# Optimization experiments

Measured on AMD Instinct MI355X. Metric: run time of the kernel, lower is better.

Reference implementation:

```python
import jax, jax.numpy as jnp
import numpy as np

N = 100000      # nodes
E = 600000      # directed edges (before self-loops)
NFEAT = 128
NHID = 128
NCLASS = 64


def setup_inputs() -> dict:
    key = jax.random.key(0)
    k1, k2, k3, k4 = jax.random.split(key, 4)
    x = jax.random.normal(k1, (N, NFEAT), dtype=jnp.float32)
    edge_index = jax.random.randint(k2, (2, E), 0, N, dtype=jnp.int32)
    # GCNConv learned params (Glorot-ish init), bias zeros as in PyG default
    W1 = jax.random.normal(k3, (NFEAT, NHID), dtype=jnp.float32) / jnp.sqrt(NFEAT)
    b1 = jnp.zeros((NHID,), dtype=jnp.float32)
    W2 = jax.random.normal(k4, (NHID, NCLASS), dtype=jnp.float32) / jnp.sqrt(NHID)
    b2 = jnp.zeros((NCLASS,), dtype=jnp.float32)
    return {"x": x, "edge_index": edge_index, "W1": W1, "b1": b1, "W2": W2, "b2": b2}


def _gcn_layer(x, src, dst, norm, W, b, n):
    # PyG GCNConv: linear transform, then normalized neighbor aggregation, then bias
    h = x @ W                                   # [N, out]
    msg = h[src] * norm[:, None]                # [E+N, out] gather + scale
    agg = jax.ops.segment_sum(msg, dst, num_segments=n)  # scatter-add
    return agg + b


def reference(x, edge_index, W1, b1, W2, b2):
    n = x.shape[0]
    # add self-loops (PyG gcn_norm default add_self_loops=True)
    loops = jnp.arange(n, dtype=edge_index.dtype)
    src = jnp.concatenate([edge_index[0], loops])
    dst = jnp.concatenate([edge_index[1], loops])
    # symmetric normalization: D^-1/2 (A+I) D^-1/2
    deg = jax.ops.segment_sum(jnp.ones_like(dst, dtype=x.dtype), dst, num_segments=n)
    d_inv_sqrt = jnp.where(deg > 0, jax.lax.rsqrt(deg), 0.0)
    norm = d_inv_sqrt[src] * d_inv_sqrt[dst]
    h = jax.nn.relu(_gcn_layer(x, src, dst, norm, W1, b1, n))
    # F.dropout with training=False is identity -> omitted in eval reference
    return _gcn_layer(h, src, dst, norm, W2, b2, n)
```

## Files before the change

kernel.cpp:

```cpp
#include <hip/hip_runtime.h>


typedef unsigned short u16;
typedef unsigned int u32;
typedef __attribute__((ext_vector_type(8))) short bf16x8;
typedef __attribute__((ext_vector_type(4))) float f32x4;

#define BSH 9
#define BMSK ((1 << BSH) - 1)
#define MAXBK 256
#define SEG 2560
#define HISTB 128

__device__ __forceinline__ u16 f2b(float f) {
  u32 u = __float_as_uint(f);
  u32 r = (u + 0x7FFFu + ((u >> 16) & 1u)) >> 16;
  return (u16)r;
}
__device__ __forceinline__ u32 pk2(float a, float b) {
  return (u32)f2b(a) | ((u32)f2b(b) << 16);
}
__device__ __forceinline__ void dec8(uint4 v, float f[8]) {
  f[0] = __uint_as_float(v.x << 16);
  f[1] = __uint_as_float(v.x & 0xFFFF0000u);
  f[2] = __uint_as_float(v.y << 16);
  f[3] = __uint_as_float(v.y & 0xFFFF0000u);
  f[4] = __uint_as_float(v.z << 16);
  f[5] = __uint_as_float(v.z & 0xFFFF0000u);
  f[6] = __uint_as_float(v.w << 16);
  f[7] = __uint_as_float(v.w & 0xFFFF0000u);
}
__device__ __forceinline__ void fma8(uint4 v, float d, float acc[8]) {
  acc[0] = fmaf(__uint_as_float(v.x << 16), d, acc[0]);
  acc[1] = fmaf(__uint_as_float(v.x & 0xFFFF0000u), d, acc[1]);
  acc[2] = fmaf(__uint_as_float(v.y << 16), d, acc[2]);
  acc[3] = fmaf(__uint_as_float(v.y & 0xFFFF0000u), d, acc[3]);
  acc[4] = fmaf(__uint_as_float(v.z << 16), d, acc[4]);
  acc[5] = fmaf(__uint_as_float(v.z & 0xFFFF0000u), d, acc[5]);
  acc[6] = fmaf(__uint_as_float(v.w << 16), d, acc[6]);
  acc[7] = fmaf(__uint_as_float(v.w & 0xFFFF0000u), d, acc[7]);
}


__global__ __launch_bounds__(256) void prep_hist_k(const void* __restrict__ W1,
                                                   const void* __restrict__ b1,
                                                   const void* __restrict__ W2,
                                                   const void* __restrict__ b2,
                                                   u16* __restrict__ W1b, u16* __restrict__ ob1,
                                                   u16* __restrict__ W2t, u16* __restrict__ ob2,
                                                   int* __restrict__ mode,
                                                   const int* __restrict__ dst,
                                                   int* __restrict__ bhist,
                                                   int E, int PREPB) {
  const int tid = threadIdx.x;

  if ((int)blockIdx.x >= PREPB) {
    __shared__ int lh[MAXBK];
    const int hb = (int)blockIdx.x - PREPB;
    for (int j = tid; j < MAXBK; j += 256) lh[j] = 0;
    __syncthreads();
    const int chunk = (E + HISTB - 1) / HISTB;
    const int e0 = hb * chunk;
    const int e1 = min(E, e0 + chunk);
    for (int e = e0 + tid; e < e1; e += 256) atomicAdd(&lh[dst[e] >> BSH], 1);
    __syncthreads();
    for (int j = tid; j < MAXBK; j += 256) {
      int v = lh[j];
      if (v) atomicAdd(&bhist[j], v);
    }
    return;
  }

  __shared__ int cnt_s;
  if (tid == 0) cnt_s = 0;
  __syncthreads();
  int c = 0;
  for (int j = tid; j < 4096; j += 256) {
    u32 e = (((const u16*)W1)[j] >> 7) & 0xFFu;
    if (e >= 100u && e <= 130u) c++;
  }
  atomicAdd(&cnt_s, c);
  __syncthreads();
  const int m = (cnt_s < 3328) ? 1 : 0;
  if (blockIdx.x == 0 && tid == 0) *mode = m;

  int i = blockIdx.x * 256 + tid;
  if (i < 24768) {
    int j = i;
    const void* src;
    u16* dstp;
    int sidx, didx;
    if (j < 16384) {
      src = W1; dstp = W1b; sidx = j; didx = j;
    } else if ((j -= 16384) < 128) {
      src = b1; dstp = ob1; sidx = j; didx = j;
    } else if ((j -= 128) < 8192) {
      int nn = j >> 7, k = j & 127;
      src = W2; dstp = W2t; sidx = k * 64 + nn; didx = j;
    } else {
      j -= 8192;
      src = b2; dstp = ob2; sidx = j; didx = j;
    }
    dstp[didx] = m ? f2b(((const float*)src)[sidx]) : ((const u16*)src)[sidx];
  }
}


__global__ __launch_bounds__(256) void part_k(const int* __restrict__ src,
                                              const int* __restrict__ dst,
                                              const int* __restrict__ bhist,
                                              int* __restrict__ boff,
                                              int2* __restrict__ tmp,
                                              int E, int NBK) {
  __shared__ int ls[SEG];
  __shared__ int ld_[SEG];
  __shared__ int lh[MAXBK];
  __shared__ int base_[MAXBK];
  __shared__ int bsl[MAXBK];
  const int tid = threadIdx.x;

  int ov = (tid < NBK) ? bhist[tid] : 0;
  bsl[tid] = ov;
  __syncthreads();
#pragma unroll
  for (int off = 1; off < 256; off <<= 1) {
    int add = (tid >= off) ? bsl[tid - off] : 0;
    __syncthreads();
    bsl[tid] += add;
    __syncthreads();
  }
  bsl[tid] -= ov;
  if (tid < MAXBK) lh[tid] = 0;
  __syncthreads();

  const int e0 = blockIdx.x * SEG;
  const int len = min(SEG, E - e0);
  for (int j = tid; j < len; j += 256) {
    int s = src[e0 + j];
    int d = dst[e0 + j];
    ls[j] = s;
    ld_[j] = d;
    atomicAdd(&lh[d >> BSH], 1);
  }
  __syncthreads();
  if (tid < NBK) {
    int hh = lh[tid];
    base_[tid] = hh ? bsl[tid] + atomicAdd(&boff[tid], hh) : 0;
    lh[tid] = 0;
  }
  __syncthreads();
  for (int j = tid; j < len; j += 256) {
    int d = ld_[j];
    int bk = d >> BSH;
    int r = atomicAdd(&lh[bk], 1);
    tmp[base_[bk] + r] = make_int2(ls[j], d);
  }
}


__global__ __launch_bounds__(256) void nbuild_k(const int2* __restrict__ tmp,
                                                const int* __restrict__ bhist,
                                                float* __restrict__ dinv,
                                                int4* __restrict__ ninfo,
                                                int* __restrict__ spI,
                                                int np, int NBK) {
  __shared__ int bsl[MAXBK];
  __shared__ int cntl[1 << BSH];
  __shared__ int curl[1 << BSH];
  __shared__ int sc2[256];
  const int tid = threadIdx.x;
  const int b = blockIdx.x;

  int ov = (tid < NBK) ? bhist[tid] : 0;
  bsl[tid] = ov;
  __syncthreads();
#pragma unroll
  for (int off = 1; off < 256; off <<= 1) {
    int add = (tid >= off) ? bsl[tid - off] : 0;
    __syncthreads();
    bsl[tid] += add;
    __syncthreads();
  }
  bsl[tid] -= ov;
  cntl[tid] = 0;
  cntl[tid + 256] = 0;
  curl[tid] = 0;
  curl[tid + 256] = 0;
  __syncthreads();

  const int bs = bsl[b];
  const int be = bs + bhist[b];
  const int lo = b << BSH;

  for (int e = bs + tid; e < be; e += 256) {
    int2 p = tmp[e];
    atomicAdd(&cntl[p.y & BMSK], 1);
  }
  __syncthreads();

  const int c0 = cntl[2 * tid];
  const int c1 = cntl[2 * tid + 1];
  const int s2 = c0 + c1;
  sc2[tid] = s2;
  __syncthreads();
#pragma unroll
  for (int off = 1; off < 256; off <<= 1) {
    int add = (tid >= off) ? sc2[tid - off] : 0;
    __syncthreads();
    sc2[tid] += add;
    __syncthreads();
  }
  const int excl = sc2[tid] - s2;
  const int e0n = excl;
  const int e1n = excl + c0;

  {
    int i0 = lo + 2 * tid;
    if (i0 < np) {
      float dv = rsqrtf((float)c0 + 1.0f);
      dinv[i0] = dv;
      ninfo[i0] = make_int4(bs + e0n, c0, __float_as_int(dv), 0);
    }
    int i1 = i0 + 1;
    if (i1 < np) {
      float dv = rsqrtf((float)c1 + 1.0f);
      dinv[i1] = dv;
      ninfo[i1] = make_int4(bs + e1n, c1, __float_as_int(dv), 0);
    }
  }
  cntl[2 * tid] = e0n;
  cntl[2 * tid + 1] = e1n;
  __syncthreads();

  for (int e = bs + tid; e < be; e += 256) {
    int2 p = tmp[e];
    int loc = p.y & BMSK;
    int r = atomicAdd(&curl[loc], 1);
    spI[bs + cntl[loc] + r] = p.x;
  }
}


__global__ __launch_bounds__(256) void gemm1_k(const void* __restrict__ Araw,
                                               const u16* __restrict__ W,
                                               u16* __restrict__ out, int M,
                                               const int* __restrict__ mode) {
  __shared__ __align__(16) u16 Wt[128 * 136];
  __shared__ __align__(16) u16 As[64 * 136];
  const int tid = threadIdx.x;
  const int mcv = *mode;

  for (int idx = tid; idx < 128 * 128; idx += 256) {
    int n = idx & 127;
    int k = idx >> 7;
    Wt[n * 136 + k] = W[k * 128 + n];
  }
  __syncthreads();

  const int wv = tid >> 6, lane = tid & 63, lr = lane & 15, lq = lane >> 4;
  const int ntiles = (M + 63) >> 6;

  for (int t = blockIdx.x; t < ntiles; t += gridDim.x) {
    const int r0 = t * 64;
    __syncthreads();
    for (int idx = tid; idx < 64 * 16; idx += 256) {
      int row = idx >> 4, c = idx & 15;
      uint4 v = make_uint4(0u, 0u, 0u, 0u);
      if (r0 + row < M) {
        if (mcv) {
          const float* xf = (const float*)Araw + (size_t)(r0 + row) * 128 + c * 8;
          float4 f0 = *(const float4*)xf;
          float4 f1 = *(const float4*)(xf + 4);
          v.x = pk2(f0.x, f0.y);
          v.y = pk2(f0.z, f0.w);
          v.z = pk2(f1.x, f1.y);
          v.w = pk2(f1.z, f1.w);
        } else {
          v = *(const uint4*)((const u16*)Araw + (size_t)(r0 + row) * 128 + c * 8);
        }
      }
      *(uint4*)&As[row * 136 + c * 8] = v;
    }
    __syncthreads();

    bf16x8 a[4];
#pragma unroll
    for (int s = 0; s < 4; ++s)
      a[s] = *(const bf16x8*)&As[(wv * 16 + lr) * 136 + s * 32 + lq * 8];

#pragma unroll
    for (int nt = 0; nt < 8; ++nt) {
      f32x4 acc = {0.f, 0.f, 0.f, 0.f};
#pragma unroll
      for (int s = 0; s < 4; ++s) {
        bf16x8 b = *(const bf16x8*)&Wt[(nt * 16 + lr) * 136 + s * 32 + lq * 8];
        acc = __builtin_amdgcn_mfma_f32_16x16x32_bf16(a[s], b, acc, 0, 0, 0);
      }
#pragma unroll
      for (int r = 0; r < 4; ++r) {
        int row = r0 + wv * 16 + lq * 4 + r;
        if (row < M) out[(size_t)row * 128 + nt * 16 + lr] = f2b(acc[r]);
      }
    }
  }
}


__global__ __launch_bounds__(256) void fusedB_k(const u16* __restrict__ h,
                                                const int* __restrict__ spI,
                                                const int4* __restrict__ ninfo,
                                                const float* __restrict__ dinv,
                                                const u16* __restrict__ b1,
                                                const u16* __restrict__ W2t,
                                                u16* __restrict__ g, int n) {
  __shared__ __align__(16) u16 As[16 * 136];
  const int tid = threadIdx.x, wv = tid >> 6, lane = tid & 63;
  const int lq = lane >> 4, lr = lane & 15;
  const int base = blockIdx.x * 16;
  const int i = base + wv * 4 + lq;
  const bool valid = (i < n);

  int start = 0, c = 0;
  float di = 0.f;
  if (valid) {
    int4 ni = ninfo[i];
    start = ni.x;
    c = ni.y;
    di = __int_as_float(ni.z);
  }
  float acc[8];
  {
    uint4 v = valid ? *(const uint4*)(h + (size_t)i * 128 + lr * 8)
                    : make_uint4(0u, 0u, 0u, 0u);
    float f[8];
    dec8(v, f);
#pragma unroll
    for (int j = 0; j < 8; ++j) acc[j] = f[j] * di;
  }
  const int bl = lq * 16;
  for (int bs = 0; __any(bs < c); bs += 16) {
    int m = c - bs;
    m = m < 0 ? 0 : (m > 16 ? 16 : m);
    int s = 0;
    float dv = 0.f;
    if (lr < m) {
      s = spI[start + bs + lr];
      dv = dinv[s];
    }
    int mmw = m;
    mmw = max(mmw, __shfl_xor(mmw, 16));
    mmw = max(mmw, __shfl_xor(mmw, 32));
    for (int e = 0; e < mmw; e += 4) {
      int s0 = __shfl(s, bl + e), s1 = __shfl(s, bl + e + 1);
      int s2 = __shfl(s, bl + e + 2), s3 = __shfl(s, bl + e + 3);
      float d0 = __shfl(dv, bl + e);
      float d1 = __shfl(dv, bl + e + 1);
      float d2 = __shfl(dv, bl + e + 2);
      float d3 = __shfl(dv, bl + e + 3);
      uint4 v0 = *(const uint4*)(h + (size_t)s0 * 128 + lr * 8);
      uint4 v1 = *(const uint4*)(h + (size_t)s1 * 128 + lr * 8);
      uint4 v2 = *(const uint4*)(h + (size_t)s2 * 128 + lr * 8);
      uint4 v3 = *(const uint4*)(h + (size_t)s3 * 128 + lr * 8);
      fma8(v0, d0, acc);
      fma8(v1, d1, acc);
      fma8(v2, d2, acc);
      fma8(v3, d3, acc);
    }
  }
  {
    uint4 bv = *(const uint4*)(b1 + lr * 8);
    float bf[8];
    dec8(bv, bf);
    float o[8];
#pragma unroll
    for (int j = 0; j < 8; ++j) o[j] = fmaxf(fmaf(acc[j], di, bf[j]), 0.f);
    uint4 ov;
    ov.x = pk2(o[0], o[1]);
    ov.y = pk2(o[2], o[3]);
    ov.z = pk2(o[4], o[5]);
    ov.w = pk2(o[6], o[7]);
    *(uint4*)&As[(wv * 4 + lq) * 136 + lr * 8] = ov;
  }
  __syncthreads();

  bf16x8 a[4];
#pragma unroll
  for (int s = 0; s < 4; ++s)
    a[s] = *(const bf16x8*)&As[lr * 136 + s * 32 + lq * 8];
  {
    const int nt = wv;
    f32x4 acc4 = {0.f, 0.f, 0.f, 0.f};
#pragma unroll
    for (int s = 0; s < 4; ++s) {
      bf16x8 b = *(const bf16x8*)&W2t[(nt * 16 + lr) * 128 + s * 32 + lq * 8];
      acc4 = __builtin_amdgcn_mfma_f32_16x16x32_bf16(a[s], b, acc4, 0, 0, 0);
    }
#pragma unroll
    for (int r = 0; r < 4; ++r) {
      int row = base + lq * 4 + r;
      if (row < n) g[(size_t)row * 64 + nt * 16 + lr] = f2b(acc4[r]);
    }
  }
}


__global__ __launch_bounds__(256) void agg2_k(const u16* __restrict__ g,
                                              const int* __restrict__ spI,
                                              const int4* __restrict__ ninfo,
                                              const float* __restrict__ dinv,
                                              const u16* __restrict__ b2,
                                              void* __restrict__ outv, int n,
                                              const int* __restrict__ mode) {
  const int lane = threadIdx.x & 63;
  const int o8 = lane >> 3, l8 = lane & 7;
  const int i = blockIdx.x * 32 + (threadIdx.x >> 6) * 8 + o8;
  const bool valid = (i < n);

  int start = 0, c = 0;
  float di = 0.f;
  if (valid) {
    int4 ni = ninfo[i];
    start = ni.x;
    c = ni.y;
    di = __int_as_float(ni.z);
  }
  float acc[8];
  {
    uint4 v = valid ? *(const uint4*)(g + (size_t)i * 64 + l8 * 8)
                    : make_uint4(0u, 0u, 0u, 0u);
    float f[8];
    dec8(v, f);
#pragma unroll
    for (int j = 0; j < 8; ++j) acc[j] = f[j] * di;
  }
  const int bl = o8 * 8;
  for (int base = 0; __any(base < c); base += 8) {
    int m = c - base;
    m = m < 0 ? 0 : (m > 8 ? 8 : m);
    int s = 0;
    float dv = 0.f;
    if (l8 < m) {
      s = spI[start + base + l8];
      dv = dinv[s];
    }
    int mmw = m;
    mmw = max(mmw, __shfl_xor(mmw, 8));
    mmw = max(mmw, __shfl_xor(mmw, 16));
    mmw = max(mmw, __shfl_xor(mmw, 32));
    for (int e = 0; e < mmw; e += 4) {
      int s0 = __shfl(s, bl + e), s1 = __shfl(s, bl + e + 1);
      int s2 = __shfl(s, bl + e + 2), s3 = __shfl(s, bl + e + 3);
      float d0 = __shfl(dv, bl + e);
      float d1 = __shfl(dv, bl + e + 1);
      float d2 = __shfl(dv, bl + e + 2);
      float d3 = __shfl(dv, bl + e + 3);
      uint4 v0 = *(const uint4*)(g + (size_t)s0 * 64 + l8 * 8);
      uint4 v1 = *(const uint4*)(g + (size_t)s1 * 64 + l8 * 8);
      uint4 v2 = *(const uint4*)(g + (size_t)s2 * 64 + l8 * 8);
      uint4 v3 = *(const uint4*)(g + (size_t)s3 * 64 + l8 * 8);
      fma8(v0, d0, acc);
      fma8(v1, d1, acc);
      fma8(v2, d2, acc);
      fma8(v3, d3, acc);
    }
  }
  if (valid) {
    uint4 bv = *(const uint4*)(b2 + l8 * 8);
    float bf[8];
    dec8(bv, bf);
    float o[8];
#pragma unroll
    for (int j = 0; j < 8; ++j) o[j] = fmaf(acc[j], di, bf[j]);
    if (*mode) {
      float* op = (float*)outv + (size_t)i * 64 + l8 * 8;
      *(float4*)op = make_float4(o[0], o[1], o[2], o[3]);
      *(float4*)(op + 4) = make_float4(o[4], o[5], o[6], o[7]);
    } else {
      uint4 ov;
      ov.x = pk2(o[0], o[1]);
      ov.y = pk2(o[2], o[3]);
      ov.z = pk2(o[4], o[5]);
      ov.w = pk2(o[6], o[7]);
      *(uint4*)((u16*)outv + (size_t)i * 64 + l8 * 8) = ov;
    }
  }
}


extern "C" void kernel_launch(void* const* d_in, const int* in_sizes, int n_in,
                              void* d_out, int out_size, void* d_ws, size_t ws_size,
                              hipStream_t stream) {
  const void* x_raw  = d_in[0];
  const int*  ei     = (const int*)d_in[1];
  const void* W1_raw = d_in[2];
  const void* b1_raw = d_in[3];
  const void* W2_raw = d_in[4];
  const void* b2_raw = d_in[5];

  const int N = in_sizes[0] / 128;
  const int E = in_sizes[1] / 2;
  const int NP = ((N + 255) / 256) * 256;
  const int NBK = (NP + (1 << BSH) - 1) >> BSH;
  const int PREPB = (24768 + 255) / 256;

  char* ws = (char*)d_ws;
  size_t off = 0;
  auto alloc = [&](size_t bytes) -> void* {
    void* p = ws + off;
    off = (off + bytes + 255) & ~(size_t)255;
    return p;
  };
  int*   mode    = (int*)alloc(4);
  int*   bz      = (int*)alloc((size_t)2 * MAXBK * 4);
  int*   bhist   = bz;
  int*   boff    = bz + MAXBK;
  float* dinv    = (float*)alloc((size_t)NP * 4);
  int4*  ninfo   = (int4*)alloc((size_t)NP * 16);
  int*   spI     = (int*)alloc((size_t)E * 4);
  int2*  tmp     = (int2*)alloc((size_t)E * 8);
  u16*   W1b     = (u16*)alloc((size_t)128 * 128 * 2);
  u16*   b1b     = (u16*)alloc(128 * 2);
  u16*   W2t     = (u16*)alloc((size_t)64 * 128 * 2);
  u16*   b2b     = (u16*)alloc(64 * 2);
  u16*   h       = (u16*)alloc((size_t)N * 128 * 2);
  u16*   g       = (u16*)alloc((size_t)N * 64 * 2);

  const int pb = (E + SEG - 1) / SEG;

  hipMemsetAsync(bz, 0, (size_t)2 * MAXBK * 4, stream);
  prep_hist_k<<<PREPB + HISTB, 256, 0, stream>>>(W1_raw, b1_raw, W2_raw, b2_raw,
                                                 W1b, b1b, W2t, b2b, mode,
                                                 ei + E, bhist, E, PREPB);
  part_k<<<pb, 256, 0, stream>>>(ei, ei + E, bhist, boff, tmp, E, NBK);
  nbuild_k<<<NBK, 256, 0, stream>>>(tmp, bhist, dinv, ninfo, spI, NP, NBK);
  gemm1_k<<<512, 256, 0, stream>>>(x_raw, W1b, h, N, mode);
  fusedB_k<<<(N + 15) / 16, 256, 0, stream>>>(h, spI, ninfo, dinv, b1b, W2t, g, N);
  agg2_k<<<(N + 31) / 32, 256, 0, stream>>>(g, spI, ninfo, dinv, b2b, d_out, N, mode);
}
```

Before: 194.4 us.

## Sort nodes by degree to balance per-wave work in aggregation kernels

Builds a degree histogram in nbuild_k, then uses extra blocks in the GEMM launch to counting-sort node ids by in-degree into a permutation. The two aggregation kernels process nodes in this permuted order, so the lanes of a wave handle nodes with similar neighbor counts and diverge less. The cost is an extra histogram and scatter pass, an indirect perm lookup, and scattered output row writes in place of contiguous ones.

```diff
diff --git a/kernel.cpp b/kernel.cpp
--- a/kernel.cpp
+++ b/kernel.cpp
@@ -11,6 +11,7 @@
 #define MAXBK 256
 #define SEG 2560
 #define HISTB 128
+#define GEMMB 512
 
 __device__ __forceinline__ u16 f2b(float f) {
   u32 u = __float_as_uint(f);
@@ -163,7 +164,8 @@
                                                 float* __restrict__ dinv,
                                                 int4* __restrict__ ninfo,
                                                 int* __restrict__ spI,
-                                                int np, int NBK) {
+                                                int* __restrict__ dhist,
+                                                int np, int n, int NBK) {
   __shared__ int bsl[MAXBK];
   __shared__ int cntl[1 << BSH];
   __shared__ int curl[1 << BSH];
@@ -220,12 +222,14 @@
       float dv = rsqrtf((float)c0 + 1.0f);
       dinv[i0] = dv;
       ninfo[i0] = make_int4(bs + e0n, c0, __float_as_int(dv), 0);
+      if (i0 < n) atomicAdd(&dhist[min(c0, 255)], 1);
     }
     int i1 = i0 + 1;
     if (i1 < np) {
       float dv = rsqrtf((float)c1 + 1.0f);
       dinv[i1] = dv;
       ninfo[i1] = make_int4(bs + e1n, c1, __float_as_int(dv), 0);
+      if (i1 < n) atomicAdd(&dhist[min(c1, 255)], 1);
     }
   }
   cntl[2 * tid] = e0n;
@@ -241,13 +245,57 @@
 }
 
 
-__global__ __launch_bounds__(256) void gemm1_k(const void* __restrict__ Araw,
-                                               const u16* __restrict__ W,
-                                               u16* __restrict__ out, int M,
-                                               const int* __restrict__ mode) {
+__global__ __launch_bounds__(256) void gemmperm_k(const void* __restrict__ Araw,
+                                                  const u16* __restrict__ W,
+                                                  u16* __restrict__ out, int M,
+                                                  const int* __restrict__ mode,
+                                                  const int4* __restrict__ ninfo,
+                                                  const int* __restrict__ dhist,
+                                                  int* __restrict__ dcur,
+                                                  int* __restrict__ perm,
+                                                  int NBp) {
   __shared__ __align__(16) u16 Wt[128 * 136];
   __shared__ __align__(16) u16 As[64 * 136];
+  __shared__ int lh[256];
+  __shared__ int base_[256];
+  __shared__ int dbase[256];
   const int tid = threadIdx.x;
+
+  if ((int)blockIdx.x < NBp) {
+    int ov = dhist[tid];
+    dbase[tid] = ov;
+    __syncthreads();
+#pragma unroll
+    for (int off = 1; off < 256; off <<= 1) {
+      int add = (tid >= off) ? dbase[tid - off] : 0;
+      __syncthreads();
+      dbase[tid] += add;
+      __syncthreads();
+    }
+    dbase[tid] -= ov;
+    lh[tid] = 0;
+    __syncthreads();
+
+    const int i = blockIdx.x * 256 + tid;
+    int c = -1;
+    if (i < M) {
+      c = min(ninfo[i].y, 255);
+      atomicAdd(&lh[c], 1);
+    }
+    __syncthreads();
+    {
+      int hh = lh[tid];
+      base_[tid] = hh ? dbase[tid] + atomicAdd(&dcur[tid], hh) : 0;
+      lh[tid] = 0;
+    }
+    __syncthreads();
+    if (i < M) {
+      int r = atomicAdd(&lh[c], 1);
+      perm[base_[c] + r] = i;
+    }
+    return;
+  }
+
   const int mcv = *mode;
 
   for (int idx = tid; idx < 128 * 128; idx += 256) {
@@ -260,7 +308,7 @@
   const int wv = tid >> 6, lane = tid & 63, lr = lane & 15, lq = lane >> 4;
   const int ntiles = (M + 63) >> 6;
 
-  for (int t = blockIdx.x; t < ntiles; t += gridDim.x) {
+  for (int t = (int)blockIdx.x - NBp; t < ntiles; t += GEMMB) {
     const int r0 = t * 64;
     __syncthreads();
     for (int idx = tid; idx < 64 * 16; idx += 256) {
@@ -310,15 +358,19 @@
                                                 const int* __restrict__ spI,
                                                 const int4* __restrict__ ninfo,
                                                 const float* __restrict__ dinv,
+                                                const int* __restrict__ perm,
                                                 const u16* __restrict__ b1,
                                                 const u16* __restrict__ W2t,
                                                 u16* __restrict__ g, int n) {
   __shared__ __align__(16) u16 As[16 * 136];
+  __shared__ int pids[16];
   const int tid = threadIdx.x, wv = tid >> 6, lane = tid & 63;
   const int lq = lane >> 4, lr = lane & 15;
   const int base = blockIdx.x * 16;
-  const int i = base + wv * 4 + lq;
-  const bool valid = (i < n);
+  const int idx = base + wv * 4 + lq;
+  const bool valid = (idx < n);
+  const int i = valid ? perm[idx] : -1;
+  if (lr == 0) pids[wv * 4 + lq] = i;
 
   int start = 0, c = 0;
   float di = 0.f;
@@ -397,8 +449,8 @@
     }
 #pragma unroll
     for (int r = 0; r < 4; ++r) {
-      int row = base + lq * 4 + r;
-      if (row < n) g[(size_t)row * 64 + nt * 16 + lr] = f2b(acc4[r]);
+      int row = pids[lq * 4 + r];
+      if (row >= 0) g[(size_t)row * 64 + nt * 16 + lr] = f2b(acc4[r]);
     }
   }
 }
@@ -408,13 +460,15 @@
                                               const int* __restrict__ spI,
                                               const int4* __restrict__ ninfo,
                                               const float* __restrict__ dinv,
+                                              const int* __restrict__ perm,
                                               const u16* __restrict__ b2,
                                               void* __restrict__ outv, int n,
                                               const int* __restrict__ mode) {
   const int lane = threadIdx.x & 63;
   const int o8 = lane >> 3, l8 = lane & 7;
-  const int i = blockIdx.x * 32 + (threadIdx.x >> 6) * 8 + o8;
-  const bool valid = (i < n);
+  const int idx = blockIdx.x * 32 + (threadIdx.x >> 6) * 8 + o8;
+  const bool valid = (idx < n);
+  const int i = valid ? perm[idx] : 0;
 
   int start = 0, c = 0;
   float di = 0.f;
@@ -502,6 +556,7 @@
   const int NP = ((N + 255) / 256) * 256;
   const int NBK = (NP + (1 << BSH) - 1) >> BSH;
   const int PREPB = (24768 + 255) / 256;
+  const int NBp = (N + 255) / 256;
 
   char* ws = (char*)d_ws;
   size_t off = 0;
@@ -511,12 +566,15 @@
     return p;
   };
   int*   mode    = (int*)alloc(4);
-  int*   bz      = (int*)alloc((size_t)2 * MAXBK * 4);
+  int*   bz      = (int*)alloc((size_t)(2 * MAXBK + 512) * 4);
   int*   bhist   = bz;
   int*   boff    = bz + MAXBK;
+  int*   dhist   = bz + 2 * MAXBK;
+  int*   dcur    = bz + 2 * MAXBK + 256;
   float* dinv    = (float*)alloc((size_t)NP * 4);
   int4*  ninfo   = (int4*)alloc((size_t)NP * 16);
   int*   spI     = (int*)alloc((size_t)E * 4);
+  int*   perm    = (int*)alloc((size_t)NP * 4);
   int2*  tmp     = (int2*)alloc((size_t)E * 8);
   u16*   W1b     = (u16*)alloc((size_t)128 * 128 * 2);
   u16*   b1b     = (u16*)alloc(128 * 2);
@@ -527,13 +585,14 @@
 
   const int pb = (E + SEG - 1) / SEG;
 
-  hipMemsetAsync(bz, 0, (size_t)2 * MAXBK * 4, stream);
+  hipMemsetAsync(bz, 0, (size_t)(2 * MAXBK + 512) * 4, stream);
   prep_hist_k<<<PREPB + HISTB, 256, 0, stream>>>(W1_raw, b1_raw, W2_raw, b2_raw,
                                                  W1b, b1b, W2t, b2b, mode,
                                                  ei + E, bhist, E, PREPB);
   part_k<<<pb, 256, 0, stream>>>(ei, ei + E, bhist, boff, tmp, E, NBK);
-  nbuild_k<<<NBK, 256, 0, stream>>>(tmp, bhist, dinv, ninfo, spI, NP, NBK);
-  gemm1_k<<<512, 256, 0, stream>>>(x_raw, W1b, h, N, mode);
-  fusedB_k<<<(N + 15) / 16, 256, 0, stream>>>(h, spI, ninfo, dinv, b1b, W2t, g, N);
-  agg2_k<<<(N + 31) / 32, 256, 0, stream>>>(g, spI, ninfo, dinv, b2b, d_out, N, mode);
-}
+  nbuild_k<<<NBK, 256, 0, stream>>>(tmp, bhist, dinv, ninfo, spI, dhist, NP, N, NBK);
+  gemmperm_k<<<NBp + GEMMB, 256, 0, stream>>>(x_raw, W1b, h, N, mode,
+                                              ninfo, dhist, dcur, perm, NBp);
+  fusedB_k<<<(N + 15) / 16, 256, 0, stream>>>(h, spI, ninfo, dinv, perm, b1b, W2t, g, N);
+  agg2_k<<<(N + 31) / 32, 256, 0, stream>>>(g, spI, ninfo, dinv, perm, b2b, d_out, N, mode);
+}
```

Result: slower. 568.4 us (+192.4%).

## Merge CSR build and first GEMM into one launch; load A fragments directly

Applied to the files above, without the earlier changes.

The neighbor-list build kernel and the first-layer GEMM are merged into a single launch. The first NBK blocks do the per-bucket CSR construction, reusing the weight shared-memory buffer as integer scratch, and the remaining blocks run the GEMM, so the two independent stages overlap and one launch is removed. The GEMM also drops the shared-memory staging of A tiles and its block barriers, loading each lane's bf16 fragments straight from global memory. The direct loads are less coalesced than the staged copy.

```diff
diff --git a/kernel.cpp b/kernel.cpp
--- a/kernel.cpp
+++ b/kernel.cpp
@@ -11,6 +11,7 @@
 #define MAXBK 256
 #define SEG 2560
 #define HISTB 128
+#define GEMMB 512
 
 __device__ __forceinline__ u16 f2b(float f) {
   u32 u = __float_as_uint(f);
@@ -158,96 +159,97 @@
 }
 
 
-__global__ __launch_bounds__(256) void nbuild_k(const int2* __restrict__ tmp,
+__global__ __launch_bounds__(256) void nbgemm_k(const int2* __restrict__ tmp,
                                                 const int* __restrict__ bhist,
                                                 float* __restrict__ dinv,
                                                 int4* __restrict__ ninfo,
                                                 int* __restrict__ spI,
-                                                int np, int NBK) {
-  __shared__ int bsl[MAXBK];
-  __shared__ int cntl[1 << BSH];
-  __shared__ int curl[1 << BSH];
-  __shared__ int sc2[256];
+                                                int np, int NBK,
+                                                const void* __restrict__ Araw,
+                                                const u16* __restrict__ W,
+                                                u16* __restrict__ hout, int M,
+                                                const int* __restrict__ mode) {
+  __shared__ __align__(16) u16 Wt[128 * 136];
   const int tid = threadIdx.x;
-  const int b = blockIdx.x;
-
-  int ov = (tid < NBK) ? bhist[tid] : 0;
-  bsl[tid] = ov;
-  __syncthreads();
-#pragma unroll
-  for (int off = 1; off < 256; off <<= 1) {
-    int add = (tid >= off) ? bsl[tid - off] : 0;
-    __syncthreads();
-    bsl[tid] += add;
-    __syncthreads();
-  }
-  bsl[tid] -= ov;
-  cntl[tid] = 0;
-  cntl[tid + 256] = 0;
-  curl[tid] = 0;
-  curl[tid + 256] = 0;
-  __syncthreads();
-
-  const int bs = bsl[b];
-  const int be = bs + bhist[b];
-  const int lo = b << BSH;
-
-  for (int e = bs + tid; e < be; e += 256) {
-    int2 p = tmp[e];
-    atomicAdd(&cntl[p.y & BMSK], 1);
-  }
-  __syncthreads();
-
-  const int c0 = cntl[2 * tid];
-  const int c1 = cntl[2 * tid + 1];
-  const int s2 = c0 + c1;
-  sc2[tid] = s2;
-  __syncthreads();
-#pragma unroll
-  for (int off = 1; off < 256; off <<= 1) {
-    int add = (tid >= off) ? sc2[tid - off] : 0;
-    __syncthreads();
-    sc2[tid] += add;
-    __syncthreads();
-  }
-  const int excl = sc2[tid] - s2;
-  const int e0n = excl;
-  const int e1n = excl + c0;
-
-  {
-    int i0 = lo + 2 * tid;
-    if (i0 < np) {
-      float dv = rsqrtf((float)c0 + 1.0f);
-      dinv[i0] = dv;
-      ninfo[i0] = make_int4(bs + e0n, c0, __float_as_int(dv), 0);
-    }
-    int i1 = i0 + 1;
-    if (i1 < np) {
-      float dv = rsqrtf((float)c1 + 1.0f);
-      dinv[i1] = dv;
-      ninfo[i1] = make_int4(bs + e1n, c1, __float_as_int(dv), 0);
-    }
-  }
-  cntl[2 * tid] = e0n;
-  cntl[2 * tid + 1] = e1n;
-  __syncthreads();
-
-  for (int e = bs + tid; e < be; e += 256) {
-    int2 p = tmp[e];
-    int loc = p.y & BMSK;
-    int r = atomicAdd(&curl[loc], 1);
-    spI[bs + cntl[loc] + r] = p.x;
-  }
-}
-
-
-__global__ __launch_bounds__(256) void gemm1_k(const void* __restrict__ Araw,
-                                               const u16* __restrict__ W,
-                                               u16* __restrict__ out, int M,
-                                               const int* __restrict__ mode) {
-  __shared__ __align__(16) u16 Wt[128 * 136];
-  __shared__ __align__(16) u16 As[64 * 136];
-  const int tid = threadIdx.x;
+
+  if ((int)blockIdx.x < NBK) {
+    int* ibuf = (int*)Wt;
+    int* bsl  = ibuf;
+    int* cntl = ibuf + 256;
+    int* curl = ibuf + 768;
+    int* sc2  = ibuf + 1280;
+    const int b = blockIdx.x;
+
+    int ov = (tid < NBK) ? bhist[tid] : 0;
+    bsl[tid] = ov;
+    __syncthreads();
+#pragma unroll
+    for (int off = 1; off < 256; off <<= 1) {
+      int add = (tid >= off) ? bsl[tid - off] : 0;
+      __syncthreads();
+      bsl[tid] += add;
+      __syncthreads();
+    }
+    bsl[tid] -= ov;
+    cntl[tid] = 0;
+    cntl[tid + 256] = 0;
+    curl[tid] = 0;
+    curl[tid + 256] = 0;
+    __syncthreads();
+
+    const int bs = bsl[b];
+    const int be = bs + bhist[b];
+    const int lo = b << BSH;
+
+    for (int e = bs + tid; e < be; e += 256) {
+      int2 p = tmp[e];
+      atomicAdd(&cntl[p.y & BMSK], 1);
+    }
+    __syncthreads();
+
+    const int c0 = cntl[2 * tid];
+    const int c1 = cntl[2 * tid + 1];
+    const int s2 = c0 + c1;
+    sc2[tid] = s2;
+    __syncthreads();
+#pragma unroll
+    for (int off = 1; off < 256; off <<= 1) {
+      int add = (tid >= off) ? sc2[tid - off] : 0;
+      __syncthreads();
+      sc2[tid] += add;
+      __syncthreads();
+    }
+    const int excl = sc2[tid] - s2;
+    const int e0n = excl;
+    const int e1n = excl + c0;
+
+    {
+      int i0 = lo + 2 * tid;
+      if (i0 < np) {
+        float dv = rsqrtf((float)c0 + 1.0f);
+        dinv[i0] = dv;
+        ninfo[i0] = make_int4(bs + e0n, c0, __float_as_int(dv), 0);
+      }
+      int i1 = i0 + 1;
+      if (i1 < np) {
+        float dv = rsqrtf((float)c1 + 1.0f);
+        dinv[i1] = dv;
+        ninfo[i1] = make_int4(bs + e1n, c1, __float_as_int(dv), 0);
+      }
+    }
+    cntl[2 * tid] = e0n;
+    cntl[2 * tid + 1] = e1n;
+    __syncthreads();
+
+    for (int e = bs + tid; e < be; e += 256) {
+      int2 p = tmp[e];
+      int loc = p.y & BMSK;
+      int r = atomicAdd(&curl[loc], 1);
+      spI[bs + cntl[loc] + r] = p.x;
+    }
+    return;
+  }
+
   const int mcv = *mode;
 
   for (int idx = tid; idx < 128 * 128; idx += 256) {
@@ -260,33 +262,35 @@
   const int wv = tid >> 6, lane = tid & 63, lr = lane & 15, lq = lane >> 4;
   const int ntiles = (M + 63) >> 6;
 
-  for (int t = blockIdx.x; t < ntiles; t += gridDim.x) {
+  for (int t = (int)blockIdx.x - NBK; t < ntiles; t += GEMMB) {
     const int r0 = t * 64;
-    __syncthreads();
-    for (int idx = tid; idx < 64 * 16; idx += 256) {
-      int row = idx >> 4, c = idx & 15;
-      uint4 v = make_uint4(0u, 0u, 0u, 0u);
-      if (r0 + row < M) {
-        if (mcv) {
-          const float* xf = (const float*)Araw + (size_t)(r0 + row) * 128 + c * 8;
-          float4 f0 = *(const float4*)xf;
-          float4 f1 = *(const float4*)(xf + 4);
-          v.x = pk2(f0.x, f0.y);
-          v.y = pk2(f0.z, f0.w);
-          v.z = pk2(f1.x, f1.y);
-          v.w = pk2(f1.z, f1.w);
-        } else {
-          v = *(const uint4*)((const u16*)Araw + (size_t)(r0 + row) * 128 + c * 8);
+    const int arow = r0 + wv * 16 + lr;
+    const bool rok = (arow < M);
+
+    bf16x8 a[4];
+    if (mcv) {
+      const float* xr = (const float*)Araw + (size_t)arow * 128 + lq * 8;
+#pragma unroll
+      for (int s = 0; s < 4; ++s) {
+        uint4 u = make_uint4(0u, 0u, 0u, 0u);
+        if (rok) {
+          float4 f0 = *(const float4*)(xr + s * 32);
+          float4 f1 = *(const float4*)(xr + s * 32 + 4);
+          u.x = pk2(f0.x, f0.y);
+          u.y = pk2(f0.z, f0.w);
+          u.z = pk2(f1.x, f1.y);
+          u.w = pk2(f1.z, f1.w);
         }
+        a[s] = *(const bf16x8*)&u;
       }
-      *(uint4*)&As[row * 136 + c * 8] = v;
-    }
-    __syncthreads();
-
-    bf16x8 a[4];
-#pragma unroll
-    for (int s = 0; s < 4; ++s)
-      a[s] = *(const bf16x8*)&As[(wv * 16 + lr) * 136 + s * 32 + lq * 8];
+    } else {
+      const u16* xr = (const u16*)Araw + (size_t)arow * 128 + lq * 8;
+#pragma unroll
+      for (int s = 0; s < 4; ++s) {
+        uint4 u = rok ? *(const uint4*)(xr + s * 32) : make_uint4(0u, 0u, 0u, 0u);
+        a[s] = *(const bf16x8*)&u;
+      }
+    }
 
 #pragma unroll
     for (int nt = 0; nt < 8; ++nt) {
@@ -299,7 +303,7 @@
 #pragma unroll
       for (int r = 0; r < 4; ++r) {
         int row = r0 + wv * 16 + lq * 4 + r;
-        if (row < M) out[(size_t)row * 128 + nt * 16 + lr] = f2b(acc[r]);
+        if (row < M) hout[(size_t)row * 128 + nt * 16 + lr] = f2b(acc[r]);
       }
     }
   }
@@ -532,8 +536,8 @@
                                                  W1b, b1b, W2t, b2b, mode,
                                                  ei + E, bhist, E, PREPB);
   part_k<<<pb, 256, 0, stream>>>(ei, ei + E, bhist, boff, tmp, E, NBK);
-  nbuild_k<<<NBK, 256, 0, stream>>>(tmp, bhist, dinv, ninfo, spI, NP, NBK);
-  gemm1_k<<<512, 256, 0, stream>>>(x_raw, W1b, h, N, mode);
+  nbgemm_k<<<NBK + GEMMB, 256, 0, stream>>>(tmp, bhist, dinv, ninfo, spI, NP, NBK,
+                                            x_raw, W1b, h, N, mode);
   fusedB_k<<<(N + 15) / 16, 256, 0, stream>>>(h, spI, ninfo, dinv, b1b, W2t, g, N);
   agg2_k<<<(N + 31) / 32, 256, 0, stream>>>(g, spI, ninfo, dinv, b2b, d_out, N, mode);
 }
```

After: 197.8 us. Within noise of the previous version (+1.7%).

## Fuse all GCN stages into one cooperative persistent kernel with overlapped GEMM

Applied to the files above, without the earlier changes.

Replaces six separate kernel launches with a single cooperative kernel of 512 blocks that uses grid-wide syncs between phases. The first GEMM (x@W1) is spread across the blocks left idle during the histogram, partition and CSR-build phases, so it overlaps the graph preprocessing. The aggregation phases now use grid-stride loops over a fixed grid. The intent is to remove launch gaps and tail idle time. In exchange it adds grid-sync overhead and reduces parallelism in the aggregation phases. It also relies on all 512 blocks being co-resident, falling back to the old launches if the cooperative launch fails.

```diff
diff --git a/kernel.cpp b/kernel.cpp
--- a/kernel.cpp
+++ b/kernel.cpp
@@ -1,5 +1,8 @@
 #include <hip/hip_runtime.h>
-
+#include <hip/hip_cooperative_groups.h>
+
+
+namespace cg = cooperative_groups;
 
 typedef unsigned short u16;
 typedef unsigned int u32;
@@ -11,6 +14,13 @@
 #define MAXBK 256
 #define SEG 2560
 #define HISTB 128
+#define PREPB 33
+#define GEMM0 (PREPB + HISTB)
+#define ROLE1 235
+#define GRID 512
+#define S1 (GRID - GEMM0)
+#define S2 (S1 + (GRID - ROLE1))
+#define STOT (S2 + (GRID - ROLE1))
 
 __device__ __forceinline__ u16 f2b(float f) {
   u32 u = __float_as_uint(f);
@@ -40,6 +50,445 @@
   acc[6] = fmaf(__uint_as_float(v.w << 16), d, acc[6]);
   acc[7] = fmaf(__uint_as_float(v.w & 0xFFFF0000u), d, acc[7]);
 }
+__device__ __forceinline__ void loadA(const void* Araw, int arow, bool rok,
+                                      int lq, int mcv, bf16x8 a[4]) {
+  if (mcv) {
+    const float* xr = (const float*)Araw + (size_t)arow * 128 + lq * 8;
+#pragma unroll
+    for (int s = 0; s < 4; ++s) {
+      uint4 u = make_uint4(0u, 0u, 0u, 0u);
+      if (rok) {
+        float4 f0 = *(const float4*)(xr + s * 32);
+        float4 f1 = *(const float4*)(xr + s * 32 + 4);
+        u.x = pk2(f0.x, f0.y);
+        u.y = pk2(f0.z, f0.w);
+        u.z = pk2(f1.x, f1.y);
+        u.w = pk2(f1.z, f1.w);
+      }
+      a[s] = *(const bf16x8*)&u;
+    }
+  } else {
+    const u16* xr = (const u16*)Araw + (size_t)arow * 128 + lq * 8;
+#pragma unroll
+    for (int s = 0; s < 4; ++s) {
+      uint4 u = rok ? *(const uint4*)(xr + s * 32) : make_uint4(0u, 0u, 0u, 0u);
+      a[s] = *(const bf16x8*)&u;
+    }
+  }
+}
+
+
+__global__ __launch_bounds__(256) void mega_k(
+    const void* __restrict__ W1, const void* __restrict__ b1,
+    const void* __restrict__ W2, const void* __restrict__ b2,
+    u16* __restrict__ b1b, u16* __restrict__ W2t, u16* __restrict__ b2b,
+    int* __restrict__ mode,
+    const int* __restrict__ esrc, const int* __restrict__ edst,
+    int* __restrict__ bhist, int* __restrict__ boff,
+    int2* __restrict__ tmp, float* __restrict__ dinv,
+    int4* __restrict__ ninfo, int* __restrict__ spI,
+    const void* __restrict__ Araw, u16* __restrict__ h,
+    u16* __restrict__ g, void* __restrict__ outv,
+    int E, int Nn, int NP, int NBK) {
+  cg::grid_group gridg = cg::this_grid();
+  __shared__ __align__(16) u16 uWt[128 * 136];
+  const int tid = threadIdx.x;
+  const int bid = blockIdx.x;
+  const int wv = tid >> 6, lane = tid & 63, lr = lane & 15, lq = lane >> 4;
+  const int ntiles = (Nn + 63) >> 6;
+  int mloc = 0;
+
+  auto do_tile = [&](int t) {
+    const int r0 = t * 64;
+    const int arow = r0 + wv * 16 + lr;
+    bf16x8 a[4];
+    loadA(Araw, arow, arow < Nn, lq, mloc, a);
+#pragma unroll
+    for (int nt = 0; nt < 8; ++nt) {
+      f32x4 acc = {0.f, 0.f, 0.f, 0.f};
+#pragma unroll
+      for (int s = 0; s < 4; ++s) {
+        bf16x8 bb = *(const bf16x8*)&uWt[(nt * 16 + lr) * 136 + s * 32 + lq * 8];
+        acc = __builtin_amdgcn_mfma_f32_16x16x32_bf16(a[s], bb, acc, 0, 0, 0);
+      }
+#pragma unroll
+      for (int r = 0; r < 4; ++r) {
+        int row = r0 + wv * 16 + lq * 4 + r;
+        if (row < Nn) h[(size_t)row * 128 + nt * 16 + lr] = f2b(acc[r]);
+      }
+    }
+  };
+
+  if (bid < PREPB) {
+    int* cnt_s = (int*)uWt;
+    if (tid == 0) *cnt_s = 0;
+    __syncthreads();
+    int c = 0;
+    for (int j = tid; j < 4096; j += 256) {
+      u32 e = (((const u16*)W1)[j] >> 7) & 0xFFu;
+      if (e >= 100u && e <= 130u) c++;
+    }
+    atomicAdd(cnt_s, c);
+    __syncthreads();
+    const int m = (*cnt_s < 3328) ? 1 : 0;
+    if (bid == 0 && tid == 0) *mode = m;
+    int i = bid * 256 + tid;
+    if (i < 8448) {
+      int j = i;
+      const void* src;
+      u16* dstp;
+      int sidx, didx;
+      if (j < 128) {
+        src = b1; dstp = b1b; sidx = j; didx = j;
+      } else if ((j -= 128) < 8192) {
+        int nn = j >> 7, k = j & 127;
+        src = W2; dstp = W2t; sidx = k * 64 + nn; didx = j;
+      } else {
+        j -= 8192;
+        src = b2; dstp = b2b; sidx = j; didx = j;
+      }
+      dstp[didx] = m ? f2b(((const float*)src)[sidx]) : ((const u16*)src)[sidx];
+    }
+  } else if (bid < GEMM0) {
+    int* lh = (int*)uWt;
+    for (int j = tid; j < MAXBK; j += 256) lh[j] = 0;
+    __syncthreads();
+    const int hb = bid - PREPB;
+    const int chunk = (E + HISTB - 1) / HISTB;
+    const int e0 = hb * chunk;
+    const int e1 = min(E, e0 + chunk);
+    for (int e = e0 + tid; e < e1; e += 256) atomicAdd(&lh[edst[e] >> BSH], 1);
+    __syncthreads();
+    for (int j = tid; j < MAXBK; j += 256) {
+      int v = lh[j];
+      if (v) atomicAdd(&bhist[j], v);
+    }
+  } else {
+    int* cnt_s = (int*)uWt;
+    if (tid == 0) *cnt_s = 0;
+    __syncthreads();
+    int c = 0;
+    for (int j = tid; j < 4096; j += 256) {
+      u32 e = (((const u16*)W1)[j] >> 7) & 0xFFu;
+      if (e >= 100u && e <= 130u) c++;
+    }
+    atomicAdd(cnt_s, c);
+    __syncthreads();
+    mloc = (*cnt_s < 3328) ? 1 : 0;
+    __syncthreads();
+    for (int idx = tid; idx < 16384; idx += 256) {
+      int nn = idx & 127, k = idx >> 7;
+      uWt[nn * 136 + k] = mloc ? f2b(((const float*)W1)[k * 128 + nn])
+                               : ((const u16*)W1)[k * 128 + nn];
+    }
+    __syncthreads();
+    for (int t = bid - GEMM0; t < ntiles; t += STOT) do_tile(t);
+  }
+  __threadfence();
+  gridg.sync();
+
+  if (bid < ROLE1) {
+    int* ls = (int*)uWt;
+    int* ld_ = ls + SEG;
+    int* lh = ld_ + SEG;
+    int* base_ = lh + MAXBK;
+    int* bsl = base_ + MAXBK;
+    const int pb = (E + SEG - 1) / SEG;
+    for (int seg = bid; seg < pb; seg += ROLE1) {
+      int ov = (tid < NBK) ? bhist[tid] : 0;
+      bsl[tid] = ov;
+      __syncthreads();
+#pragma unroll
+      for (int off = 1; off < 256; off <<= 1) {
+        int add = (tid >= off) ? bsl[tid - off] : 0;
+        __syncthreads();
+        bsl[tid] += add;
+        __syncthreads();
+      }
+      bsl[tid] -= ov;
+      if (tid < MAXBK) lh[tid] = 0;
+      __syncthreads();
+
+      const int e0 = seg * SEG;
+      const int len = min(SEG, E - e0);
+      for (int j = tid; j < len; j += 256) {
+        int s = esrc[e0 + j];
+        int d = edst[e0 + j];
+        ls[j] = s;
+        ld_[j] = d;
+        atomicAdd(&lh[d >> BSH], 1);
+      }
+      __syncthreads();
+      if (tid < NBK) {
+        int hh = lh[tid];
+        base_[tid] = hh ? bsl[tid] + atomicAdd(&boff[tid], hh) : 0;
+        lh[tid] = 0;
+      }
+      __syncthreads();
+      for (int j = tid; j < len; j += 256) {
+        int d = ld_[j];
+        int bk = d >> BSH;
+        int r = atomicAdd(&lh[bk], 1);
+        tmp[base_[bk] + r] = make_int2(ls[j], d);
+      }
+      __syncthreads();
+    }
+  } else {
+    for (int t = S1 + (bid - ROLE1); t < ntiles; t += STOT) do_tile(t);
+  }
+  __threadfence();
+  gridg.sync();
+
+  if (bid < NBK) {
+    int* bsl = (int*)uWt;
+    int* cntl = bsl + MAXBK;
+    int* curl = cntl + 512;
+    int* sc2 = curl + 512;
+    int ov = (tid < NBK) ? bhist[tid] : 0;
+    bsl[tid] = ov;
+    __syncthreads();
+#pragma unroll
+    for (int off = 1; off < 256; off <<= 1) {
+      int add = (tid >= off) ? bsl[tid - off] : 0;
+      __syncthreads();
+      bsl[tid] += add;
+      __syncthreads();
+    }
+    bsl[tid] -= ov;
+    cntl[tid] = 0;
+    cntl[tid + 256] = 0;
+    curl[tid] = 0;
+    curl[tid + 256] = 0;
+    __syncthreads();
+
+    const int bs = bsl[bid];
+    const int be = bs + bhist[bid];
+    const int lo = bid << BSH;
+
+    for (int e = bs + tid; e < be; e += 256) {
+      int2 p = tmp[e];
+      atomicAdd(&cntl[p.y & BMSK], 1);
+    }
+    __syncthreads();
+
+    const int c0 = cntl[2 * tid];
+    const int c1 = cntl[2 * tid + 1];
+    const int s2 = c0 + c1;
+    sc2[tid] = s2;
+    __syncthreads();
+#pragma unroll
+    for (int off = 1; off < 256; off <<= 1) {
+      int add = (tid >= off) ? sc2[tid - off] : 0;
+      __syncthreads();
+      sc2[tid] += add;
+      __syncthreads();
+    }
+    const int excl = sc2[tid] - s2;
+    const int e0n = excl;
+    const int e1n = excl + c0;
+
+    {
+      int i0 = lo + 2 * tid;
+      if (i0 < NP) {
+        float dv = rsqrtf((float)c0 + 1.0f);
+        dinv[i0] = dv;
+        ninfo[i0] = make_int4(bs + e0n, c0, __float_as_int(dv), 0);
+      }
+      int i1 = i0 + 1;
+      if (i1 < NP) {
+        float dv = rsqrtf((float)c1 + 1.0f);
+        dinv[i1] = dv;
+        ninfo[i1] = make_int4(bs + e1n, c1, __float_as_int(dv), 0);
+      }
+    }
+    cntl[2 * tid] = e0n;
+    cntl[2 * tid + 1] = e1n;
+    __syncthreads();
+
+    for (int e = bs + tid; e < be; e += 256) {
+      int2 p = tmp[e];
+      int loc = p.y & BMSK;
+      int r = atomicAdd(&curl[loc], 1);
+      spI[bs + cntl[loc] + r] = p.x;
+    }
+  } else if (bid >= ROLE1) {
+    for (int t = S2 + (bid - ROLE1); t < ntiles; t += STOT) do_tile(t);
+  }
+  __threadfence();
+  gridg.sync();
+
+  {
+    u16* As = uWt;
+    const int bl = lq * 16;
+    for (int grp = bid; grp * 16 < Nn; grp += GRID) {
+      const int base = grp * 16;
+      const int i = base + wv * 4 + lq;
+      const bool valid = (i < Nn);
+
+      int start = 0, c = 0;
+      float di = 0.f;
+      if (valid) {
+        int4 ni = ninfo[i];
+        start = ni.x;
+        c = ni.y;
+        di = __int_as_float(ni.z);
+      }
+      float acc[8];
+      {
+        uint4 v = valid ? *(const uint4*)(h + (size_t)i * 128 + lr * 8)
+                        : make_uint4(0u, 0u, 0u, 0u);
+        float f[8];
+        dec8(v, f);
+#pragma unroll
+        for (int j = 0; j < 8; ++j) acc[j] = f[j] * di;
+      }
+      for (int bs = 0; __any(bs < c); bs += 16) {
+        int m = c - bs;
+        m = m < 0 ? 0 : (m > 16 ? 16 : m);
+        int s = 0;
+        float dv = 0.f;
+        if (lr < m) {
+          s = spI[start + bs + lr];
+          dv = dinv[s];
+        }
+        int mmw = m;
+        mmw = max(mmw, __shfl_xor(mmw, 16));
+        mmw = max(mmw, __shfl_xor(mmw, 32));
+        for (int e = 0; e < mmw; e += 4) {
+          int s0 = __shfl(s, bl + e), s1 = __shfl(s, bl + e + 1);
+          int s2 = __shfl(s, bl + e + 2), s3 = __shfl(s, bl + e + 3);
+          float d0 = __shfl(dv, bl + e);
+          float d1 = __shfl(dv, bl + e + 1);
+          float d2 = __shfl(dv, bl + e + 2);
+          float d3 = __shfl(dv, bl + e + 3);
+          uint4 v0 = *(const uint4*)(h + (size_t)s0 * 128 + lr * 8);
+          uint4 v1 = *(const uint4*)(h + (size_t)s1 * 128 + lr * 8);
+          uint4 v2 = *(const uint4*)(h + (size_t)s2 * 128 + lr * 8);
+          uint4 v3 = *(const uint4*)(h + (size_t)s3 * 128 + lr * 8);
+          fma8(v0, d0, acc);
+          fma8(v1, d1, acc);
+          fma8(v2, d2, acc);
+          fma8(v3, d3, acc);
+        }
+      }
+      {
+        uint4 bv = *(const uint4*)(b1b + lr * 8);
+        float bf[8];
+        dec8(bv, bf);
+        float o[8];
+#pragma unroll
+        for (int j = 0; j < 8; ++j) o[j] = fmaxf(fmaf(acc[j], di, bf[j]), 0.f);
+        uint4 ov;
+        ov.x = pk2(o[0], o[1]);
+        ov.y = pk2(o[2], o[3]);
+        ov.z = pk2(o[4], o[5]);
+        ov.w = pk2(o[6], o[7]);
+        *(uint4*)&As[(wv * 4 + lq) * 136 + lr * 8] = ov;
+      }
+      __syncthreads();
+
+      bf16x8 a[4];
+#pragma unroll
+      for (int s = 0; s < 4; ++s)
+        a[s] = *(const bf16x8*)&As[lr * 136 + s * 32 + lq * 8];
+      {
+        const int nt = wv;
+        f32x4 acc4 = {0.f, 0.f, 0.f, 0.f};
+#pragma unroll
+        for (int s = 0; s < 4; ++s) {
+          bf16x8 bb = *(const bf16x8*)&W2t[(nt * 16 + lr) * 128 + s * 32 + lq * 8];
+          acc4 = __builtin_amdgcn_mfma_f32_16x16x32_bf16(a[s], bb, acc4, 0, 0, 0);
+        }
+#pragma unroll
+        for (int r = 0; r < 4; ++r) {
+          int row = base + lq * 4 + r;
+          if (row < Nn) g[(size_t)row * 64 + nt * 16 + lr] = f2b(acc4[r]);
+        }
+      }
+      __syncthreads();
+    }
+  }
+  __threadfence();
+  gridg.sync();
+
+  {
+    const int o8 = lane >> 3, l8 = lane & 7;
+    const int bl = o8 * 8;
+    const int modev = *mode;
+    for (int grp = bid; grp * 32 < Nn; grp += GRID) {
+      const int i = grp * 32 + (tid >> 6) * 8 + o8;
+      const bool valid = (i < Nn);
+
+      int start = 0, c = 0;
+      float di = 0.f;
+      if (valid) {
+        int4 ni = ninfo[i];
+        start = ni.x;
+        c = ni.y;
+        di = __int_as_float(ni.z);
+      }
+      float acc[8];
+      {
+        uint4 v = valid ? *(const uint4*)(g + (size_t)i * 64 + l8 * 8)
+                        : make_uint4(0u, 0u, 0u, 0u);
+        float f[8];
+        dec8(v, f);
+#pragma unroll
+        for (int j = 0; j < 8; ++j) acc[j] = f[j] * di;
+      }
+      for (int base = 0; __any(base < c); base += 8) {
+        int m = c - base;
+        m = m < 0 ? 0 : (m > 8 ? 8 : m);
+        int s = 0;
+        float dv = 0.f;
+        if (l8 < m) {
+          s = spI[start + base + l8];
+          dv = dinv[s];
+        }
+        int mmw = m;
+        mmw = max(mmw, __shfl_xor(mmw, 8));
+        mmw = max(mmw, __shfl_xor(mmw, 16));
+        mmw = max(mmw, __shfl_xor(mmw, 32));
+        for (int e = 0; e < mmw; e += 4) {
+          int s0 = __shfl(s, bl + e), s1 = __shfl(s, bl + e + 1);
+          int s2 = __shfl(s, bl + e + 2), s3 = __shfl(s, bl + e + 3);
+          float d0 = __shfl(dv, bl + e);
+          float d1 = __shfl(dv, bl + e + 1);
+          float d2 = __shfl(dv, bl + e + 2);
+          float d3 = __shfl(dv, bl + e + 3);
+          uint4 v0 = *(const uint4*)(g + (size_t)s0 * 64 + l8 * 8);
+          uint4 v1 = *(const uint4*)(g + (size_t)s1 * 64 + l8 * 8);
+          uint4 v2 = *(const uint4*)(g + (size_t)s2 * 64 + l8 * 8);
+          uint4 v3 = *(const uint4*)(g + (size_t)s3 * 64 + l8 * 8);
+          fma8(v0, d0, acc);
+          fma8(v1, d1, acc);
+          fma8(v2, d2, acc);
+          fma8(v3, d3, acc);
+        }
+      }
+      if (valid) {
+        uint4 bv = *(const uint4*)(b2b + l8 * 8);
+        float bf[8];
+        dec8(bv, bf);
+        float o[8];
+#pragma unroll
+        for (int j = 0; j < 8; ++j) o[j] = fmaf(acc[j], di, bf[j]);
+        if (modev) {
+          float* op = (float*)outv + (size_t)i * 64 + l8 * 8;
+          *(float4*)op = make_float4(o[0], o[1], o[2], o[3]);
+          *(float4*)(op + 4) = make_float4(o[4], o[5], o[6], o[7]);
+        } else {
+          uint4 ov;
+          ov.x = pk2(o[0], o[1]);
+          ov.y = pk2(o[2], o[3]);
+          ov.z = pk2(o[4], o[5]);
+          ov.w = pk2(o[6], o[7]);
+          *(uint4*)((u16*)outv + (size_t)i * 64 + l8 * 8) = ov;
+        }
+      }
+    }
+  }
+}
 
 
 __global__ __launch_bounds__(256) void prep_hist_k(const void* __restrict__ W1,
@@ -51,12 +500,12 @@
                                                    int* __restrict__ mode,
                                                    const int* __restrict__ dst,
                                                    int* __restrict__ bhist,
-                                                   int E, int PREPB) {
+                                                   int E, int PREPBn) {
   const int tid = threadIdx.x;
 
-  if ((int)blockIdx.x >= PREPB) {
+  if ((int)blockIdx.x >= PREPBn) {
     __shared__ int lh[MAXBK];
-    const int hb = (int)blockIdx.x - PREPB;
+    const int hb = (int)blockIdx.x - PREPBn;
     for (int j = tid; j < MAXBK; j += 256) lh[j] = 0;
     __syncthreads();
     const int chunk = (E + HISTB - 1) / HISTB;
@@ -105,7 +554,6 @@
   }
 }
 
-
 __global__ __launch_bounds__(256) void part_k(const int* __restrict__ src,
                                               const int* __restrict__ dst,
                                               const int* __restrict__ bhist,
@@ -157,7 +605,6 @@
   }
 }
 
-
 __global__ __launch_bounds__(256) void nbuild_k(const int2* __restrict__ tmp,
                                                 const int* __restrict__ bhist,
                                                 float* __restrict__ dinv,
@@ -239,7 +686,6 @@
     spI[bs + cntl[loc] + r] = p.x;
   }
 }
-
 
 __global__ __launch_bounds__(256) void gemm1_k(const void* __restrict__ Araw,
                                                const u16* __restrict__ W,
@@ -304,7 +750,6 @@
     }
   }
 }
-
 
 __global__ __launch_bounds__(256) void fusedB_k(const u16* __restrict__ h,
                                                 const int* __restrict__ spI,
@@ -402,7 +847,6 @@
     }
   }
 }
-
 
 __global__ __launch_bounds__(256) void agg2_k(const u16* __restrict__ g,
                                               const int* __restrict__ spI,
@@ -501,7 +945,6 @@
   const int E = in_sizes[1] / 2;
   const int NP = ((N + 255) / 256) * 256;
   const int NBK = (NP + (1 << BSH) - 1) >> BSH;
-  const int PREPB = (24768 + 255) / 256;
 
   char* ws = (char*)d_ws;
   size_t off = 0;
@@ -525,15 +968,30 @@
   u16*   h       = (u16*)alloc((size_t)N * 128 * 2);
   u16*   g       = (u16*)alloc((size_t)N * 64 * 2);
 
-  const int pb = (E + SEG - 1) / SEG;
-
   hipMemsetAsync(bz, 0, (size_t)2 * MAXBK * 4, stream);
-  prep_hist_k<<<PREPB + HISTB, 256, 0, stream>>>(W1_raw, b1_raw, W2_raw, b2_raw,
-                                                 W1b, b1b, W2t, b2b, mode,
-                                                 ei + E, bhist, E, PREPB);
-  part_k<<<pb, 256, 0, stream>>>(ei, ei + E, bhist, boff, tmp, E, NBK);
-  nbuild_k<<<NBK, 256, 0, stream>>>(tmp, bhist, dinv, ninfo, spI, NP, NBK);
-  gemm1_k<<<512, 256, 0, stream>>>(x_raw, W1b, h, N, mode);
-  fusedB_k<<<(N + 15) / 16, 256, 0, stream>>>(h, spI, ninfo, dinv, b1b, W2t, g, N);
-  agg2_k<<<(N + 31) / 32, 256, 0, stream>>>(g, spI, ninfo, dinv, b2b, d_out, N, mode);
-}
+
+  const int* esrc = ei;
+  const int* edst = ei + E;
+  void* kargs[] = {
+    (void*)&W1_raw, (void*)&b1_raw, (void*)&W2_raw, (void*)&b2_raw,
+    (void*)&b1b, (void*)&W2t, (void*)&b2b, (void*)&mode,
+    (void*)&esrc, (void*)&edst, (void*)&bhist, (void*)&boff,
+    (void*)&tmp, (void*)&dinv, (void*)&ninfo, (void*)&spI,
+    (void*)&x_raw, (void*)&h, (void*)&g, (void*)&d_out,
+    (void*)&E, (void*)&N, (void*)&NP, (void*)&NBK
+  };
+  hipError_t cerr = hipLaunchCooperativeKernel((const void*)mega_k, dim3(GRID),
+                                               dim3(256), kargs, 0, stream);
+  if (cerr != hipSuccess) {
+    const int PREPBn = (24768 + 255) / 256;
+    const int pb = (E + SEG - 1) / SEG;
+    prep_hist_k<<<PREPBn + HISTB, 256, 0, stream>>>(W1_raw, b1_raw, W2_raw, b2_raw,
+                                                    W1b, b1b, W2t, b2b, mode,
+                                                    ei + E, bhist, E, PREPBn);
+    part_k<<<pb, 256, 0, stream>>>(ei, ei + E, bhist, boff, tmp, E, NBK);
+    nbuild_k<<<NBK, 256, 0, stream>>>(tmp, bhist, dinv, ninfo, spI, NP, NBK);
+    gemm1_k<<<512, 256, 0, stream>>>(x_raw, W1b, h, N, mode);
+    fusedB_k<<<(N + 15) / 16, 256, 0, stream>>>(h, spI, ninfo, dinv, b1b, W2t, g, N);
+    agg2_k<<<(N + 31) / 32, 256, 0, stream>>>(g, spI, ninfo, dinv, b2b, d_out, N, mode);
+  }
+}
```

After: 735.5 us. +278.4%, slower.
